# Kernel tuning notes

Measured on AMD Instinct MI355X. Metric: run time of the kernel, lower is better.

Reference implementation:

```python
import jax, jax.numpy as jnp
import numpy as np

N = 2_000_000
NUM_IN = 9
F1, F2 = 32, 64
NUM_SEG = 100_000
EPS = 1e-5


def setup_inputs() -> dict:
    key = jax.random.key(0)
    ks = jax.random.split(key, 10)
    points = jax.random.normal(ks[0], (N, NUM_IN), dtype=jnp.float32)
    inverse_indices = jax.random.randint(ks[1], (N,), 0, NUM_SEG, dtype=jnp.int64)
    w1 = jax.random.normal(ks[2], (NUM_IN, F1), dtype=jnp.float32) / np.sqrt(NUM_IN)
    b1 = jax.random.normal(ks[3], (F1,), dtype=jnp.float32) * 0.01
    g1 = jnp.ones((F1,), jnp.float32)
    be1 = jnp.zeros((F1,), jnp.float32)
    w2 = jax.random.normal(ks[4], (F1, F2), dtype=jnp.float32) / np.sqrt(F1)
    b2 = jax.random.normal(ks[5], (F2,), dtype=jnp.float32) * 0.01
    g2 = jnp.ones((F2,), jnp.float32)
    be2 = jnp.zeros((F2,), jnp.float32)
    return {
        "points": points, "inverse_indices": inverse_indices, "num_segments": NUM_SEG,
        "w1": w1, "b1": b1, "g1": g1, "be1": be1,
        "w2": w2, "b2": b2, "g2": g2, "be2": be2,
    }


def _linear_bn_relu(x, w, b, gamma, beta):
    # Linear -> BatchNorm1d (training-mode batch stats, biased var, eps=1e-5) -> ReLU
    h = x @ w + b
    mean = h.mean(axis=0)
    var = h.var(axis=0)  # biased, matches torch BN normalization
    h = (h - mean) * jax.lax.rsqrt(var + EPS) * gamma + beta
    return jax.nn.relu(h)


def reference(points, inverse_indices, num_segments, w1, b1, g1, be1, w2, b2, g2, be2):
    feat = _linear_bn_relu(points, w1, b1, g1, be1)
    feat = _linear_bn_relu(feat, w2, b2, g2, be2)
    # scatter_max over dim 0; torch_scatter zero-initializes empty segments,
    # and post-ReLU features are >= 0, so clamp -inf (empty) to 0.
    seg = jax.ops.segment_max(feat, inverse_indices, num_segments=num_segments)
    return jnp.maximum(seg, 0.0)
```

## Files before the change

kernel.cpp:

```cpp
#include <hip/hip_runtime.h>

#define EPS 1e-5f
#define NIN 9
#define F1 32
#define F2 64
#define NMOM 45
#define ROWB 80
#define SHIFT 7
#define NSEGB 128
#define NBMAX 1024
#define BT_MAIN 2048
#define BT_FB 8192
#define WSTRIDE 68

#define WS_S    0
#define WS_M    16
#define WS_S2   64
#define WS_SS2  128
#define WS_SC1  192
#define WS_SH1  224
#define WS_W1P  256
#define WS_SC2  544
#define WS_SH2  608

typedef __attribute__((ext_vector_type(8))) short bf16x8;
typedef __attribute__((ext_vector_type(4))) float f32x4;

__device__ __forceinline__ unsigned int f2bf(float f) {
    unsigned int u = __float_as_uint(f);
    return (u + 0x7fffu + ((u >> 16) & 1u)) >> 16;
}
__device__ __forceinline__ unsigned int pack2(float lo, float hi) {
    return f2bf(lo) | (f2bf(hi) << 16);
}

__global__ __launch_bounds__(256, 4) void moments_kernel(
    const float* __restrict__ pts, const int* __restrict__ idx,
    float* __restrict__ ws, int* __restrict__ histc, int N, int nb)
{
    __shared__ int lhist[NBMAX];
    __shared__ float red[64];
    for (int t = threadIdx.x; t < nb; t += 256) lhist[t] = 0;

    float S[NIN], M[NMOM];
#pragma unroll
    for (int k = 0; k < NIN; ++k) S[k] = 0.f;
#pragma unroll
    for (int m = 0; m < NMOM; ++m) M[m] = 0.f;
    __syncthreads();

    const int stride = gridDim.x * blockDim.x;
    for (int i = blockIdx.x * blockDim.x + threadIdx.x; i < N; i += stride) {
        const float* p = pts + (size_t)i * NIN;
        atomicAdd(&lhist[idx[i] >> SHIFT], 1);
        float x[NIN];
#pragma unroll
        for (int k = 0; k < NIN; ++k) x[k] = p[k];
        int m = 0;
#pragma unroll
        for (int k = 0; k < NIN; ++k) {
            S[k] += x[k];
#pragma unroll
            for (int l = k; l < NIN; ++l) { M[m] = fmaf(x[k], x[l], M[m]); ++m; }
        }
    }
#pragma unroll
    for (int off = 32; off > 0; off >>= 1) {
#pragma unroll
        for (int k = 0; k < NIN; ++k) S[k] += __shfl_xor(S[k], off, 64);
#pragma unroll
        for (int m = 0; m < NMOM; ++m) M[m] += __shfl_xor(M[m], off, 64);
    }
    if (threadIdx.x < 64) red[threadIdx.x] = 0.f;
    __syncthreads();
    if ((threadIdx.x & 63) == 0) {
#pragma unroll
        for (int k = 0; k < NIN; ++k) atomicAdd(&red[WS_S + k], S[k]);
#pragma unroll
        for (int m = 0; m < NMOM; ++m) atomicAdd(&red[WS_M + m], M[m]);
    }
    __syncthreads();
    if (threadIdx.x < 64) atomicAdd(&ws[threadIdx.x], red[threadIdx.x]);
    for (int t = threadIdx.x; t < nb; t += 256)
        if (lhist[t] > 0) atomicAdd(&histc[t], lhist[t]);
}

__global__ void scan_coarse_kernel(const int* __restrict__ histc,
                                   int* __restrict__ offsets,
                                   int* __restrict__ cursor, int nb)
{
    __shared__ int part[256];
    const int tid = threadIdx.x;
    int v[4];
    int sum = 0;
    const int base = tid * 4;
#pragma unroll
    for (int j = 0; j < 4; ++j) {
        const int i = base + j;
        v[j] = (i < nb) ? histc[i] : 0;
        sum += v[j];
    }
    part[tid] = sum;
    __syncthreads();
    for (int d = 1; d < 256; d <<= 1) {
        int t = (tid >= d) ? part[tid - d] : 0;
        __syncthreads();
        part[tid] += t;
        __syncthreads();
    }
    int pre = part[tid] - sum;
#pragma unroll
    for (int j = 0; j < 4; ++j) {
        const int i = base + j;
        if (i < nb) { offsets[i] = pre; cursor[i] = pre; }
        pre += v[j];
    }
    if (tid == 255) offsets[nb] = part[255];
}

__global__ void finalize1_kernel(
    const float* __restrict__ w1, const float* __restrict__ b1,
    const float* __restrict__ g1, const float* __restrict__ be1,
    float* __restrict__ ws, float invN)
{
    __shared__ float sc1s[F1];
    const int j = threadIdx.x;
    if (j < F1) {
        float W[NIN];
        float P = 0.f;
#pragma unroll
        for (int k = 0; k < NIN; ++k) {
            W[k] = w1[k * F1 + j];
            P = fmaf(ws[WS_S + k], W[k], P);
        }
        float Q = 0.f;
        int m = 0;
#pragma unroll
        for (int k = 0; k < NIN; ++k) {
            Q = fmaf(ws[WS_M + m], W[k] * W[k], Q); ++m;
#pragma unroll
            for (int l = k + 1; l < NIN; ++l) {
                Q = fmaf(2.f * ws[WS_M + m], W[k] * W[l], Q); ++m;
            }
        }
        const float b = b1[j];
        const float mean = fmaf(P, invN, b);
        const float Eh2 = fmaf(fmaf(2.f * b, P, Q), invN, b * b);
        const float var = Eh2 - mean * mean;
        const float sc = g1[j] * rsqrtf(var + EPS);
        ws[WS_SC1 + j] = sc;
        ws[WS_SH1 + j] = be1[j] - mean * sc;
        sc1s[j] = sc;
    }
    __syncthreads();
    for (int m = threadIdx.x; m < NIN * F1; m += blockDim.x)
        ws[WS_W1P + m] = w1[m] * sc1s[m & (F1 - 1)];
}

__global__ void finalize2_kernel(
    const float* __restrict__ g2, const float* __restrict__ be2,
    const float* __restrict__ b2, float* __restrict__ ws, float invN, float padf)
{
    const int j = threadIdx.x;
    if (j < F2) {
        const float b = b2[j];
        const float S  = ws[WS_S2 + j]  - padf * b;
        const float SS = ws[WS_SS2 + j] - padf * b * b;
        const float mean = S * invN;
        const float var  = SS * invN - mean * mean;
        const float sc   = g2[j] * rsqrtf(var + EPS);
        ws[WS_SC2 + j] = sc;
        ws[WS_SH2 + j] = be2[j] - mean * sc;
    }
}

__device__ __forceinline__ void f1_row_bf16(
    const float* __restrict__ p, const float* __restrict__ wl,
    const float* __restrict__ sh1, unsigned int* __restrict__ pk )
{
    float x[NIN];
#pragma unroll
    for (int k = 0; k < NIN; ++k) x[k] = p[k];
#pragma unroll
    for (int fc = 0; fc < 4; ++fc) {
        float h[8];
#pragma unroll
        for (int jj = 0; jj < 8; ++jj) h[jj] = sh1[fc * 8 + jj];
#pragma unroll
        for (int k = 0; k < NIN; ++k) {
            const float xv = x[k];
#pragma unroll
            for (int jj = 0; jj < 8; ++jj)
                h[jj] = fmaf(xv, wl[k * F1 + fc * 8 + jj], h[jj]);
        }
#pragma unroll
        for (int jj = 0; jj < 4; ++jj)
            pk[fc * 4 + jj] = pack2(fmaxf(h[2 * jj], 0.f), fmaxf(h[2 * jj + 1], 0.f));
    }
}

__global__ __launch_bounds__(256, 3) void binf1_kernel(
    const float* __restrict__ pts, const int* __restrict__ idx,
    const float* __restrict__ w2, const float* __restrict__ b2,
    float* __restrict__ ws, int* __restrict__ cursor,
    uint4* __restrict__ f1buf, int* __restrict__ fseg, int N, int nb)
{
    __shared__ int lcnt[NBMAX], runbase[NBMAX];
    __shared__ __align__(16) unsigned char stag[4][64 * ROWB];
    __shared__ float red[2 * F2];

    const int tid = threadIdx.x;
    const int t0 = blockIdx.x * BT_MAIN;
    const int lane = tid & 63, wv = tid >> 6;
    const int quad = lane >> 4, m16 = lane & 15;

    for (int t = tid; t < nb; t += 256) lcnt[t] = 0;
    __syncthreads();
#pragma unroll
    for (int r = 0; r < BT_MAIN / 256; ++r) {
        const int i = t0 + r * 256 + tid;
        if (i < N) atomicAdd(&lcnt[idx[i] >> SHIFT], 1);
    }
    __syncthreads();
    for (int t = tid; t < nb; t += 256) {
        const int c = lcnt[t];
        if (c > 0) runbase[t] = atomicAdd(&cursor[t], c);
        lcnt[t] = 0;
    }
    __syncthreads();

    bf16x8 bfr[4];
#pragma unroll
    for (int nt = 0; nt < 4; ++nt)
#pragma unroll
        for (int j = 0; j < 8; ++j)
            bfr[nt][j] = (short)f2bf(w2[(quad * 8 + j) * F2 + nt * 16 + m16]);
    float b2f[4];
#pragma unroll
    for (int nt = 0; nt < 4; ++nt) b2f[nt] = b2[nt * 16 + m16];

    const float* wl  = ws + WS_W1P;
    const float* sh1 = ws + WS_SH1;
    const f32x4 zero = {0.f, 0.f, 0.f, 0.f};
    float s[4] = {0.f, 0.f, 0.f, 0.f}, ss[4] = {0.f, 0.f, 0.f, 0.f};
    unsigned char* myst = stag[wv];

#pragma unroll 1
    for (int r = 0; r < BT_MAIN / 256; ++r) {
        const int cstart = t0 + r * 256 + wv * 64;
        if (cstart >= N) continue;
        const int i = cstart + lane;
        unsigned int pk[16];
        if (i < N) {
            f1_row_bf16(pts + (size_t)i * NIN, wl, sh1, pk);
        } else {
#pragma unroll
            for (int q = 0; q < 16; ++q) pk[q] = 0u;
        }
        uint4* wrow = (uint4*)(myst + lane * ROWB);
#pragma unroll
        for (int cidx = 0; cidx < 4; ++cidx)
            wrow[cidx] = make_uint4(pk[4*cidx+0], pk[4*cidx+1], pk[4*cidx+2], pk[4*cidx+3]);

        if (i < N) {
            const int sg = idx[i];
            const int bb = sg >> SHIFT;
            const int p = runbase[bb] + atomicAdd(&lcnt[bb], 1);
            uint4* dst = f1buf + (size_t)p * 4;
            dst[0] = make_uint4(pk[0],  pk[1],  pk[2],  pk[3]);
            dst[1] = make_uint4(pk[4],  pk[5],  pk[6],  pk[7]);
            dst[2] = make_uint4(pk[8],  pk[9],  pk[10], pk[11]);
            dst[3] = make_uint4(pk[12], pk[13], pk[14], pk[15]);
            fseg[p] = sg;
        }

        bf16x8 afr[4];
#pragma unroll
        for (int mt = 0; mt < 4; ++mt)
            afr[mt] = *(const bf16x8*)(myst + (mt * 16 + m16) * ROWB + quad * 16);
#pragma unroll
        for (int mt = 0; mt < 4; ++mt) {
#pragma unroll
            for (int nt = 0; nt < 4; ++nt) {
                f32x4 d = __builtin_amdgcn_mfma_f32_16x16x32_bf16(afr[mt], bfr[nt], zero, 0, 0, 0);
#pragma unroll
                for (int rr = 0; rr < 4; ++rr) {
                    const float v = d[rr] + b2f[nt];
                    s[nt] += v;
                    ss[nt] = fmaf(v, v, ss[nt]);
                }
            }
        }
    }

#pragma unroll
    for (int off = 16; off < 64; off <<= 1)
#pragma unroll
        for (int nt = 0; nt < 4; ++nt) {
            s[nt]  += __shfl_xor(s[nt], off, 64);
            ss[nt] += __shfl_xor(ss[nt], off, 64);
        }
    if (tid < 2 * F2) red[tid] = 0.f;
    __syncthreads();
    if (quad == 0) {
#pragma unroll
        for (int nt = 0; nt < 4; ++nt) {
            atomicAdd(&red[nt * 16 + m16], s[nt]);
            atomicAdd(&red[F2 + nt * 16 + m16], ss[nt]);
        }
    }
    __syncthreads();
    if (tid < F2) {
        atomicAdd(&ws[WS_S2 + tid],  red[tid]);
        atomicAdd(&ws[WS_SS2 + tid], red[F2 + tid]);
    }
}

__global__ __launch_bounds__(256, 3) void bucket_scatter_kernel(
    const uint4* __restrict__ f1buf, const int* __restrict__ fseg,
    const float* __restrict__ w2, const float* __restrict__ b2,
    const float* __restrict__ ws, const int* __restrict__ offsets,
    unsigned int* __restrict__ out, int nseg)
{
    __shared__ unsigned int win[NSEGB * WSTRIDE];
    __shared__ int segl[4][64];

    const int b = blockIdx.x;
    const int start = offsets[b], end = offsets[b + 1];
    const int tid = threadIdx.x;
    const int lane = tid & 63, wv = tid >> 6;
    const int quad = lane >> 4, m16 = lane & 15;

    for (int t = tid; t < NSEGB * WSTRIDE; t += 256) win[t] = 0u;

    bf16x8 bfr[4];
#pragma unroll
    for (int nt = 0; nt < 4; ++nt)
#pragma unroll
        for (int j = 0; j < 8; ++j)
            bfr[nt][j] = (short)f2bf(w2[(quad * 8 + j) * F2 + nt * 16 + m16]);
    float sc2f[4], shb[4];
#pragma unroll
    for (int nt = 0; nt < 4; ++nt) {
        const int f = nt * 16 + m16;
        sc2f[nt] = ws[WS_SC2 + f];
        shb[nt]  = fmaf(b2[f], sc2f[nt], ws[WS_SH2 + f]);
    }
    const f32x4 zero = {0.f, 0.f, 0.f, 0.f};
    __syncthreads();

    const int segbase = b << SHIFT;
    const int nch = (end - start + 63) >> 6;
    const bf16x8* fb = (const bf16x8*)f1buf;
    for (int c = wv; c < nch; c += 4) {
        const int cbase = start + c * 64;
        segl[wv][lane] = (cbase + lane < end) ? (fseg[cbase + lane] - segbase) : -1;
        bf16x8 afr[4];
#pragma unroll
        for (int mt = 0; mt < 4; ++mt) {
            const int ri = cbase + mt * 16 + m16;
            if (ri < end) {
                afr[mt] = fb[(size_t)ri * 4 + quad];
            } else {
#pragma unroll
                for (int j = 0; j < 8; ++j) afr[mt][j] = 0;
            }
        }
#pragma unroll
        for (int mt = 0; mt < 4; ++mt) {
            f32x4 d[4];
#pragma unroll
            for (int nt = 0; nt < 4; ++nt)
                d[nt] = __builtin_amdgcn_mfma_f32_16x16x32_bf16(afr[mt], bfr[nt], zero, 0, 0, 0);
#pragma unroll
            for (int rr = 0; rr < 4; ++rr) {
                const int sl = segl[wv][mt * 16 + quad * 4 + rr];
                if (sl >= 0) {
#pragma unroll
                    for (int nt = 0; nt < 4; ++nt) {
                        const float v = fmaf(d[nt][rr], sc2f[nt], shb[nt]);
                        if (v > 0.f)
                            atomicMax(&win[sl * WSTRIDE + nt * 16 + m16], __float_as_uint(v));
                    }
                }
            }
        }
    }
    __syncthreads();
    const int rows = min(NSEGB, nseg - segbase);
    for (int t = tid; t < rows * 64; t += 256)
        out[(size_t)(segbase + (t >> 6)) * 64 + (t & 63)] = win[(t >> 6) * WSTRIDE + (t & 63)];
}

__global__ __launch_bounds__(256) void binning_fb_kernel(
    const int* __restrict__ idx, int* __restrict__ cursor,
    int* __restrict__ sidx, int* __restrict__ fseg, int N, int nb)
{
    __shared__ int lcnt[NBMAX];
    __shared__ int runbase[NBMAX];
    const int tid = threadIdx.x;
    const int t0 = blockIdx.x * BT_FB;
    for (int t = tid; t < nb; t += 256) lcnt[t] = 0;
    __syncthreads();
#pragma unroll 4
    for (int r = 0; r < BT_FB / 256; ++r) {
        const int i = t0 + r * 256 + tid;
        if (i < N) atomicAdd(&lcnt[idx[i] >> SHIFT], 1);
    }
    __syncthreads();
    for (int t = tid; t < nb; t += 256) {
        const int c = lcnt[t];
        if (c > 0) runbase[t] = atomicAdd(&cursor[t], c);
        lcnt[t] = 0;
    }
    __syncthreads();
#pragma unroll 4
    for (int r = 0; r < BT_FB / 256; ++r) {
        const int i = t0 + r * 256 + tid;
        if (i < N) {
            const int sg = idx[i];
            const int bb = sg >> SHIFT;
            const int p = runbase[bb] + atomicAdd(&lcnt[bb], 1);
            sidx[p] = i;
            fseg[p] = sg;
        }
    }
}

__global__ __launch_bounds__(256, 3) void stats2_kernel(
    const float* __restrict__ pts, const float* __restrict__ w2,
    const float* __restrict__ b2, float* __restrict__ ws, int N)
{
    __shared__ __align__(16) unsigned char stag[4][64 * ROWB];
    __shared__ float red[2 * F2];

    const int lane = threadIdx.x & 63, wv = threadIdx.x >> 6;
    const int quad = lane >> 4, m16 = lane & 15;

    bf16x8 bfr[4];
#pragma unroll
    for (int nt = 0; nt < 4; ++nt)
#pragma unroll
        for (int j = 0; j < 8; ++j)
            bfr[nt][j] = (short)f2bf(w2[(quad * 8 + j) * F2 + nt * 16 + m16]);
    float b2f[4];
#pragma unroll
    for (int nt = 0; nt < 4; ++nt) b2f[nt] = b2[nt * 16 + m16];

    const float* wl  = ws + WS_W1P;
    const float* sh1 = ws + WS_SH1;
    const f32x4 zero = {0.f, 0.f, 0.f, 0.f};
    float s[4] = {0.f, 0.f, 0.f, 0.f}, ss[4] = {0.f, 0.f, 0.f, 0.f};

    unsigned char* myst = stag[wv];
    const int nchunks = (N + 63) / 64;
    for (int c = blockIdx.x * 4 + wv; c < nchunks; c += gridDim.x * 4) {
        const int i = c * 64 + lane;
        unsigned int pk[16];
        if (i < N) {
            f1_row_bf16(pts + (size_t)i * NIN, wl, sh1, pk);
        } else {
#pragma unroll
            for (int q = 0; q < 16; ++q) pk[q] = 0u;
        }
        uint4* wrow = (uint4*)(myst + lane * ROWB);
#pragma unroll
        for (int cidx = 0; cidx < 4; ++cidx)
            wrow[cidx] = make_uint4(pk[4*cidx+0], pk[4*cidx+1], pk[4*cidx+2], pk[4*cidx+3]);

        bf16x8 afr[4];
#pragma unroll
        for (int mt = 0; mt < 4; ++mt)
            afr[mt] = *(const bf16x8*)(myst + (mt * 16 + m16) * ROWB + quad * 16);
#pragma unroll
        for (int mt = 0; mt < 4; ++mt) {
#pragma unroll
            for (int nt = 0; nt < 4; ++nt) {
                f32x4 d = __builtin_amdgcn_mfma_f32_16x16x32_bf16(afr[mt], bfr[nt], zero, 0, 0, 0);
#pragma unroll
                for (int rr = 0; rr < 4; ++rr) {
                    const float v = d[rr] + b2f[nt];
                    s[nt] += v;
                    ss[nt] = fmaf(v, v, ss[nt]);
                }
            }
        }
    }
#pragma unroll
    for (int off = 16; off < 64; off <<= 1)
#pragma unroll
        for (int nt = 0; nt < 4; ++nt) {
            s[nt]  += __shfl_xor(s[nt], off, 64);
            ss[nt] += __shfl_xor(ss[nt], off, 64);
        }
    if (threadIdx.x < 2 * F2) red[threadIdx.x] = 0.f;
    __syncthreads();
    if (quad == 0) {
#pragma unroll
        for (int nt = 0; nt < 4; ++nt) {
            atomicAdd(&red[nt * 16 + m16], s[nt]);
            atomicAdd(&red[F2 + nt * 16 + m16], ss[nt]);
        }
    }
    __syncthreads();
    if (threadIdx.x < F2) {
        atomicAdd(&ws[WS_S2 + threadIdx.x],  red[threadIdx.x]);
        atomicAdd(&ws[WS_SS2 + threadIdx.x], red[F2 + threadIdx.x]);
    }
}

__global__ __launch_bounds__(256, 2) void bucket_scatter_gather_kernel(
    const float* __restrict__ pts, const int* __restrict__ sidx,
    const int* __restrict__ fseg, const float* __restrict__ w2,
    const float* __restrict__ b2, const float* __restrict__ ws,
    const int* __restrict__ offsets, unsigned int* __restrict__ out, int nseg)
{
    __shared__ unsigned int win[NSEGB * WSTRIDE];
    __shared__ __align__(16) unsigned char stag[4][64 * ROWB];
    __shared__ int segl[4][64];

    const int b = blockIdx.x;
    const int start = offsets[b], end = offsets[b + 1];
    const int tid = threadIdx.x;
    const int lane = tid & 63, wv = tid >> 6;
    const int quad = lane >> 4, m16 = lane & 15;

    for (int t = tid; t < NSEGB * WSTRIDE; t += 256) win[t] = 0u;

    bf16x8 bfr[4];
#pragma unroll
    for (int nt = 0; nt < 4; ++nt)
#pragma unroll
        for (int j = 0; j < 8; ++j)
            bfr[nt][j] = (short)f2bf(w2[(quad * 8 + j) * F2 + nt * 16 + m16]);
    float sc2f[4], shb[4];
#pragma unroll
    for (int nt = 0; nt < 4; ++nt) {
        const int f = nt * 16 + m16;
        sc2f[nt] = ws[WS_SC2 + f];
        shb[nt]  = fmaf(b2[f], sc2f[nt], ws[WS_SH2 + f]);
    }
    const float* wl  = ws + WS_W1P;
    const float* sh1 = ws + WS_SH1;
    const f32x4 zero = {0.f, 0.f, 0.f, 0.f};
    __syncthreads();

    const int segbase = b << SHIFT;
    const int nch = (end - start + 63) >> 6;
    unsigned char* myst = stag[wv];
    for (int c = wv; c < nch; c += 4) {
        const int cbase = start + c * 64;
        const int sp = cbase + lane;
        unsigned int pk[16];
        int sl = -1;
        if (sp < end) {
            f1_row_bf16(pts + (size_t)sidx[sp] * NIN, wl, sh1, pk);
            sl = fseg[sp] - segbase;
        } else {
#pragma unroll
            for (int q = 0; q < 16; ++q) pk[q] = 0u;
        }
        segl[wv][lane] = sl;
        uint4* wrow = (uint4*)(myst + lane * ROWB);
#pragma unroll
        for (int cidx = 0; cidx < 4; ++cidx)
            wrow[cidx] = make_uint4(pk[4*cidx+0], pk[4*cidx+1], pk[4*cidx+2], pk[4*cidx+3]);

        bf16x8 afr[4];
#pragma unroll
        for (int mt = 0; mt < 4; ++mt)
            afr[mt] = *(const bf16x8*)(myst + (mt * 16 + m16) * ROWB + quad * 16);
#pragma unroll
        for (int mt = 0; mt < 4; ++mt) {
            f32x4 d[4];
#pragma unroll
            for (int nt = 0; nt < 4; ++nt)
                d[nt] = __builtin_amdgcn_mfma_f32_16x16x32_bf16(afr[mt], bfr[nt], zero, 0, 0, 0);
#pragma unroll
            for (int rr = 0; rr < 4; ++rr) {
                const int sl2 = segl[wv][mt * 16 + quad * 4 + rr];
                if (sl2 >= 0) {
#pragma unroll
                    for (int nt = 0; nt < 4; ++nt) {
                        const float v = fmaf(d[nt][rr], sc2f[nt], shb[nt]);
                        if (v > 0.f)
                            atomicMax(&win[sl2 * WSTRIDE + nt * 16 + m16], __float_as_uint(v));
                    }
                }
            }
        }
    }
    __syncthreads();
    const int rows = min(NSEGB, nseg - segbase);
    for (int t = tid; t < rows * 64; t += 256)
        out[(size_t)(segbase + (t >> 6)) * 64 + (t & 63)] = win[(t >> 6) * WSTRIDE + (t & 63)];
}

extern "C" void kernel_launch(void* const* d_in, const int* in_sizes, int n_in,
                              void* d_out, int out_size, void* d_ws, size_t ws_size,
                              hipStream_t stream)
{
    const float* pts = (const float*)d_in[0];
    const int*   idx = (const int*)d_in[1];
    const float* w1  = (const float*)d_in[3];
    const float* b1  = (const float*)d_in[4];
    const float* g1  = (const float*)d_in[5];
    const float* be1 = (const float*)d_in[6];
    const float* w2  = (const float*)d_in[7];
    const float* b2  = (const float*)d_in[8];
    const float* g2  = (const float*)d_in[9];
    const float* be2 = (const float*)d_in[10];

    const int N = in_sizes[0] / NIN;
    const int nseg = out_size / F2;
    const int nb = (nseg + NSEGB - 1) >> SHIFT;
    const float invN = 1.0f / (float)N;
    const float padf = (float)((64 - (N & 63)) & 63);

    char* base = (char*)d_ws;
    const size_t f1bytes = (size_t)N * 64;
    const size_t need_main = f1bytes + 4096
                           + ((size_t)NBMAX + NBMAX + 1 + NBMAX + N) * sizeof(int) + 256;

    if (ws_size >= need_main) {
        uint4* f1buf   = (uint4*)base;
        float* ws      = (float*)(base + f1bytes);
        int*   histc   = (int*)(base + f1bytes + 4096);
        int*   offsets = histc + NBMAX;
        int*   cursor  = offsets + NBMAX + 1;
        int*   fseg    = cursor + NBMAX;

        hipMemsetAsync(ws, 0, 192 * sizeof(float), stream);
        hipMemsetAsync(histc, 0, NBMAX * sizeof(int), stream);

        moments_kernel<<<1024, 256, 0, stream>>>(pts, idx, ws, histc, N, nb);
        finalize1_kernel<<<1, 320, 0, stream>>>(w1, b1, g1, be1, ws, invN);
        scan_coarse_kernel<<<1, 256, 0, stream>>>(histc, offsets, cursor, nb);
        binf1_kernel<<<(N + BT_MAIN - 1) / BT_MAIN, 256, 0, stream>>>(
            pts, idx, w2, b2, ws, cursor, f1buf, fseg, N, nb);
        finalize2_kernel<<<1, 64, 0, stream>>>(g2, be2, b2, ws, invN, padf);
        bucket_scatter_kernel<<<nb, 256, 0, stream>>>(
            f1buf, fseg, w2, b2, ws, offsets, (unsigned int*)d_out, nseg);
    } else {
        float* ws      = (float*)base;
        int*   histc   = (int*)(base + 4096);
        int*   offsets = histc + NBMAX;
        int*   cursor  = offsets + NBMAX + 1;
        int*   sidx    = cursor + NBMAX;
        int*   fseg    = sidx + N;

        hipMemsetAsync(ws, 0, 192 * sizeof(float), stream);
        hipMemsetAsync(histc, 0, NBMAX * sizeof(int), stream);

        moments_kernel<<<1024, 256, 0, stream>>>(pts, idx, ws, histc, N, nb);
        finalize1_kernel<<<1, 320, 0, stream>>>(w1, b1, g1, be1, ws, invN);
        scan_coarse_kernel<<<1, 256, 0, stream>>>(histc, offsets, cursor, nb);
        binning_fb_kernel<<<(N + BT_FB - 1) / BT_FB, 256, 0, stream>>>(
            idx, cursor, sidx, fseg, N, nb);
        stats2_kernel<<<1024, 256, 0, stream>>>(pts, w2, b2, ws, N);
        finalize2_kernel<<<1, 64, 0, stream>>>(g2, be2, b2, ws, invN, padf);
        bucket_scatter_gather_kernel<<<nb, 256, 0, stream>>>(
            pts, sidx, fseg, w2, b2, ws, offsets, (unsigned int*)d_out, nseg);
    }
}
```

Measured before the change: 329.6 us.

## Split fused binning/F1 kernel into coalesced F1 write plus separate pair binning

The fused kernel that computed layer-1 features and scattered them into bucket order is split into two kernels. One writes bf16 F1 rows in original order with coalesced stores while accumulating layer-2 stats. The other bins (index, segment) pairs into a packed int2 array. The bucket scatter kernel now gathers F1 rows by index, so the scattered 64-byte writes become random 64-byte reads, plus an extra pass over idx and an extra launch.

```diff
diff --git a/kernel.cpp b/kernel.cpp
--- a/kernel.cpp
+++ b/kernel.cpp
@@ -9,8 +9,7 @@
 #define SHIFT 7
 #define NSEGB 128
 #define NBMAX 1024
-#define BT_MAIN 2048
-#define BT_FB 8192
+#define BT_BIN 8192
 #define WSTRIDE 68
 
 #define WS_S    0
@@ -199,237 +198,10 @@
     }
 }
 
-__global__ __launch_bounds__(256, 3) void binf1_kernel(
-    const float* __restrict__ pts, const int* __restrict__ idx,
-    const float* __restrict__ w2, const float* __restrict__ b2,
-    float* __restrict__ ws, int* __restrict__ cursor,
-    uint4* __restrict__ f1buf, int* __restrict__ fseg, int N, int nb)
-{
-    __shared__ int lcnt[NBMAX], runbase[NBMAX];
-    __shared__ __align__(16) unsigned char stag[4][64 * ROWB];
-    __shared__ float red[2 * F2];
-
-    const int tid = threadIdx.x;
-    const int t0 = blockIdx.x * BT_MAIN;
-    const int lane = tid & 63, wv = tid >> 6;
-    const int quad = lane >> 4, m16 = lane & 15;
-
-    for (int t = tid; t < nb; t += 256) lcnt[t] = 0;
-    __syncthreads();
-#pragma unroll
-    for (int r = 0; r < BT_MAIN / 256; ++r) {
-        const int i = t0 + r * 256 + tid;
-        if (i < N) atomicAdd(&lcnt[idx[i] >> SHIFT], 1);
-    }
-    __syncthreads();
-    for (int t = tid; t < nb; t += 256) {
-        const int c = lcnt[t];
-        if (c > 0) runbase[t] = atomicAdd(&cursor[t], c);
-        lcnt[t] = 0;
-    }
-    __syncthreads();
-
-    bf16x8 bfr[4];
-#pragma unroll
-    for (int nt = 0; nt < 4; ++nt)
-#pragma unroll
-        for (int j = 0; j < 8; ++j)
-            bfr[nt][j] = (short)f2bf(w2[(quad * 8 + j) * F2 + nt * 16 + m16]);
-    float b2f[4];
-#pragma unroll
-    for (int nt = 0; nt < 4; ++nt) b2f[nt] = b2[nt * 16 + m16];
-
-    const float* wl  = ws + WS_W1P;
-    const float* sh1 = ws + WS_SH1;
-    const f32x4 zero = {0.f, 0.f, 0.f, 0.f};
-    float s[4] = {0.f, 0.f, 0.f, 0.f}, ss[4] = {0.f, 0.f, 0.f, 0.f};
-    unsigned char* myst = stag[wv];
-
-#pragma unroll 1
-    for (int r = 0; r < BT_MAIN / 256; ++r) {
-        const int cstart = t0 + r * 256 + wv * 64;
-        if (cstart >= N) continue;
-        const int i = cstart + lane;
-        unsigned int pk[16];
-        if (i < N) {
-            f1_row_bf16(pts + (size_t)i * NIN, wl, sh1, pk);
-        } else {
-#pragma unroll
-            for (int q = 0; q < 16; ++q) pk[q] = 0u;
-        }
-        uint4* wrow = (uint4*)(myst + lane * ROWB);
-#pragma unroll
-        for (int cidx = 0; cidx < 4; ++cidx)
-            wrow[cidx] = make_uint4(pk[4*cidx+0], pk[4*cidx+1], pk[4*cidx+2], pk[4*cidx+3]);
-
-        if (i < N) {
-            const int sg = idx[i];
-            const int bb = sg >> SHIFT;
-            const int p = runbase[bb] + atomicAdd(&lcnt[bb], 1);
-            uint4* dst = f1buf + (size_t)p * 4;
-            dst[0] = make_uint4(pk[0],  pk[1],  pk[2],  pk[3]);
-            dst[1] = make_uint4(pk[4],  pk[5],  pk[6],  pk[7]);
-            dst[2] = make_uint4(pk[8],  pk[9],  pk[10], pk[11]);
-            dst[3] = make_uint4(pk[12], pk[13], pk[14], pk[15]);
-            fseg[p] = sg;
-        }
-
-        bf16x8 afr[4];
-#pragma unroll
-        for (int mt = 0; mt < 4; ++mt)
-            afr[mt] = *(const bf16x8*)(myst + (mt * 16 + m16) * ROWB + quad * 16);
-#pragma unroll
-        for (int mt = 0; mt < 4; ++mt) {
-#pragma unroll
-            for (int nt = 0; nt < 4; ++nt) {
-                f32x4 d = __builtin_amdgcn_mfma_f32_16x16x32_bf16(afr[mt], bfr[nt], zero, 0, 0, 0);
-#pragma unroll
-                for (int rr = 0; rr < 4; ++rr) {
-                    const float v = d[rr] + b2f[nt];
-                    s[nt] += v;
-                    ss[nt] = fmaf(v, v, ss[nt]);
-                }
-            }
-        }
-    }
-
-#pragma unroll
-    for (int off = 16; off < 64; off <<= 1)
-#pragma unroll
-        for (int nt = 0; nt < 4; ++nt) {
-            s[nt]  += __shfl_xor(s[nt], off, 64);
-            ss[nt] += __shfl_xor(ss[nt], off, 64);
-        }
-    if (tid < 2 * F2) red[tid] = 0.f;
-    __syncthreads();
-    if (quad == 0) {
-#pragma unroll
-        for (int nt = 0; nt < 4; ++nt) {
-            atomicAdd(&red[nt * 16 + m16], s[nt]);
-            atomicAdd(&red[F2 + nt * 16 + m16], ss[nt]);
-        }
-    }
-    __syncthreads();
-    if (tid < F2) {
-        atomicAdd(&ws[WS_S2 + tid],  red[tid]);
-        atomicAdd(&ws[WS_SS2 + tid], red[F2 + tid]);
-    }
-}
-
-__global__ __launch_bounds__(256, 3) void bucket_scatter_kernel(
-    const uint4* __restrict__ f1buf, const int* __restrict__ fseg,
-    const float* __restrict__ w2, const float* __restrict__ b2,
-    const float* __restrict__ ws, const int* __restrict__ offsets,
-    unsigned int* __restrict__ out, int nseg)
-{
-    __shared__ unsigned int win[NSEGB * WSTRIDE];
-    __shared__ int segl[4][64];
-
-    const int b = blockIdx.x;
-    const int start = offsets[b], end = offsets[b + 1];
-    const int tid = threadIdx.x;
-    const int lane = tid & 63, wv = tid >> 6;
-    const int quad = lane >> 4, m16 = lane & 15;
-
-    for (int t = tid; t < NSEGB * WSTRIDE; t += 256) win[t] = 0u;
-
-    bf16x8 bfr[4];
-#pragma unroll
-    for (int nt = 0; nt < 4; ++nt)
-#pragma unroll
-        for (int j = 0; j < 8; ++j)
-            bfr[nt][j] = (short)f2bf(w2[(quad * 8 + j) * F2 + nt * 16 + m16]);
-    float sc2f[4], shb[4];
-#pragma unroll
-    for (int nt = 0; nt < 4; ++nt) {
-        const int f = nt * 16 + m16;
-        sc2f[nt] = ws[WS_SC2 + f];
-        shb[nt]  = fmaf(b2[f], sc2f[nt], ws[WS_SH2 + f]);
-    }
-    const f32x4 zero = {0.f, 0.f, 0.f, 0.f};
-    __syncthreads();
-
-    const int segbase = b << SHIFT;
-    const int nch = (end - start + 63) >> 6;
-    const bf16x8* fb = (const bf16x8*)f1buf;
-    for (int c = wv; c < nch; c += 4) {
-        const int cbase = start + c * 64;
-        segl[wv][lane] = (cbase + lane < end) ? (fseg[cbase + lane] - segbase) : -1;
-        bf16x8 afr[4];
-#pragma unroll
-        for (int mt = 0; mt < 4; ++mt) {
-            const int ri = cbase + mt * 16 + m16;
-            if (ri < end) {
-                afr[mt] = fb[(size_t)ri * 4 + quad];
-            } else {
-#pragma unroll
-                for (int j = 0; j < 8; ++j) afr[mt][j] = 0;
-            }
-        }
-#pragma unroll
-        for (int mt = 0; mt < 4; ++mt) {
-            f32x4 d[4];
-#pragma unroll
-            for (int nt = 0; nt < 4; ++nt)
-                d[nt] = __builtin_amdgcn_mfma_f32_16x16x32_bf16(afr[mt], bfr[nt], zero, 0, 0, 0);
-#pragma unroll
-            for (int rr = 0; rr < 4; ++rr) {
-                const int sl = segl[wv][mt * 16 + quad * 4 + rr];
-                if (sl >= 0) {
-#pragma unroll
-                    for (int nt = 0; nt < 4; ++nt) {
-                        const float v = fmaf(d[nt][rr], sc2f[nt], shb[nt]);
-                        if (v > 0.f)
-                            atomicMax(&win[sl * WSTRIDE + nt * 16 + m16], __float_as_uint(v));
-                    }
-                }
-            }
-        }
-    }
-    __syncthreads();
-    const int rows = min(NSEGB, nseg - segbase);
-    for (int t = tid; t < rows * 64; t += 256)
-        out[(size_t)(segbase + (t >> 6)) * 64 + (t & 63)] = win[(t >> 6) * WSTRIDE + (t & 63)];
-}
-
-__global__ __launch_bounds__(256) void binning_fb_kernel(
-    const int* __restrict__ idx, int* __restrict__ cursor,
-    int* __restrict__ sidx, int* __restrict__ fseg, int N, int nb)
-{
-    __shared__ int lcnt[NBMAX];
-    __shared__ int runbase[NBMAX];
-    const int tid = threadIdx.x;
-    const int t0 = blockIdx.x * BT_FB;
-    for (int t = tid; t < nb; t += 256) lcnt[t] = 0;
-    __syncthreads();
-#pragma unroll 4
-    for (int r = 0; r < BT_FB / 256; ++r) {
-        const int i = t0 + r * 256 + tid;
-        if (i < N) atomicAdd(&lcnt[idx[i] >> SHIFT], 1);
-    }
-    __syncthreads();
-    for (int t = tid; t < nb; t += 256) {
-        const int c = lcnt[t];
-        if (c > 0) runbase[t] = atomicAdd(&cursor[t], c);
-        lcnt[t] = 0;
-    }
-    __syncthreads();
-#pragma unroll 4
-    for (int r = 0; r < BT_FB / 256; ++r) {
-        const int i = t0 + r * 256 + tid;
-        if (i < N) {
-            const int sg = idx[i];
-            const int bb = sg >> SHIFT;
-            const int p = runbase[bb] + atomicAdd(&lcnt[bb], 1);
-            sidx[p] = i;
-            fseg[p] = sg;
-        }
-    }
-}
-
-__global__ __launch_bounds__(256, 3) void stats2_kernel(
+__global__ __launch_bounds__(256, 3) void f1stats_kernel(
     const float* __restrict__ pts, const float* __restrict__ w2,
-    const float* __restrict__ b2, float* __restrict__ ws, int N)
+    const float* __restrict__ b2, float* __restrict__ ws,
+    uint4* __restrict__ f1buf, int N)
 {
     __shared__ __align__(16) unsigned char stag[4][64 * ROWB];
     __shared__ float red[2 * F2];
@@ -468,6 +240,14 @@
         for (int cidx = 0; cidx < 4; ++cidx)
             wrow[cidx] = make_uint4(pk[4*cidx+0], pk[4*cidx+1], pk[4*cidx+2], pk[4*cidx+3]);
 
+        if (i < N) {
+            uint4* dst = f1buf + (size_t)i * 4;
+            dst[0] = make_uint4(pk[0],  pk[1],  pk[2],  pk[3]);
+            dst[1] = make_uint4(pk[4],  pk[5],  pk[6],  pk[7]);
+            dst[2] = make_uint4(pk[8],  pk[9],  pk[10], pk[11]);
+            dst[3] = make_uint4(pk[12], pk[13], pk[14], pk[15]);
+        }
+
         bf16x8 afr[4];
 #pragma unroll
         for (int mt = 0; mt < 4; ++mt)
@@ -486,6 +266,7 @@
             }
         }
     }
+
 #pragma unroll
     for (int off = 16; off < 64; off <<= 1)
 #pragma unroll
@@ -509,11 +290,210 @@
     }
 }
 
+__global__ __launch_bounds__(256) void binning_kernel(
+    const int* __restrict__ idx, int* __restrict__ cursor,
+    int2* __restrict__ pair, int N, int nb)
+{
+    __shared__ int lcnt[NBMAX];
+    __shared__ int runbase[NBMAX];
+    const int tid = threadIdx.x;
+    const int t0 = blockIdx.x * BT_BIN;
+    for (int t = tid; t < nb; t += 256) lcnt[t] = 0;
+    __syncthreads();
+#pragma unroll 4
+    for (int r = 0; r < BT_BIN / 256; ++r) {
+        const int i = t0 + r * 256 + tid;
+        if (i < N) atomicAdd(&lcnt[idx[i] >> SHIFT], 1);
+    }
+    __syncthreads();
+    for (int t = tid; t < nb; t += 256) {
+        const int c = lcnt[t];
+        if (c > 0) runbase[t] = atomicAdd(&cursor[t], c);
+        lcnt[t] = 0;
+    }
+    __syncthreads();
+#pragma unroll 4
+    for (int r = 0; r < BT_BIN / 256; ++r) {
+        const int i = t0 + r * 256 + tid;
+        if (i < N) {
+            const int sg = idx[i];
+            const int bb = sg >> SHIFT;
+            const int p = runbase[bb] + atomicAdd(&lcnt[bb], 1);
+            pair[p] = make_int2(i, sg);
+        }
+    }
+}
+
+__global__ __launch_bounds__(256, 3) void bucket_scatter_kernel(
+    const uint4* __restrict__ f1buf, const int2* __restrict__ pair,
+    const float* __restrict__ w2, const float* __restrict__ b2,
+    const float* __restrict__ ws, const int* __restrict__ offsets,
+    unsigned int* __restrict__ out, int nseg)
+{
+    __shared__ unsigned int win[NSEGB * WSTRIDE];
+    __shared__ int2 prl[4][64];
+
+    const int b = blockIdx.x;
+    const int start = offsets[b], end = offsets[b + 1];
+    const int tid = threadIdx.x;
+    const int lane = tid & 63, wv = tid >> 6;
+    const int quad = lane >> 4, m16 = lane & 15;
+
+    for (int t = tid; t < NSEGB * WSTRIDE; t += 256) win[t] = 0u;
+
+    bf16x8 bfr[4];
+#pragma unroll
+    for (int nt = 0; nt < 4; ++nt)
+#pragma unroll
+        for (int j = 0; j < 8; ++j)
+            bfr[nt][j] = (short)f2bf(w2[(quad * 8 + j) * F2 + nt * 16 + m16]);
+    float sc2f[4], shb[4];
+#pragma unroll
+    for (int nt = 0; nt < 4; ++nt) {
+        const int f = nt * 16 + m16;
+        sc2f[nt] = ws[WS_SC2 + f];
+        shb[nt]  = fmaf(b2[f], sc2f[nt], ws[WS_SH2 + f]);
+    }
+    const f32x4 zero = {0.f, 0.f, 0.f, 0.f};
+    __syncthreads();
+
+    const int segbase = b << SHIFT;
+    const int nch = (end - start + 63) >> 6;
+    const bf16x8* fb = (const bf16x8*)f1buf;
+    for (int c = wv; c < nch; c += 4) {
+        const int cbase = start + c * 64;
+        const int sp = cbase + lane;
+        int2 pr = make_int2(0, -1);
+        if (sp < end) {
+            pr = pair[sp];
+            pr.y -= segbase;
+        }
+        prl[wv][lane] = pr;
+
+        bf16x8 afr[4];
+#pragma unroll
+        for (int mt = 0; mt < 4; ++mt) {
+            if (cbase + mt * 16 + m16 < end) {
+                const int gi = prl[wv][mt * 16 + m16].x;
+                afr[mt] = fb[(size_t)gi * 4 + quad];
+            } else {
+#pragma unroll
+                for (int j = 0; j < 8; ++j) afr[mt][j] = 0;
+            }
+        }
+#pragma unroll
+        for (int mt = 0; mt < 4; ++mt) {
+            f32x4 d[4];
+#pragma unroll
+            for (int nt = 0; nt < 4; ++nt)
+                d[nt] = __builtin_amdgcn_mfma_f32_16x16x32_bf16(afr[mt], bfr[nt], zero, 0, 0, 0);
+#pragma unroll
+            for (int rr = 0; rr < 4; ++rr) {
+                const int sl = prl[wv][mt * 16 + quad * 4 + rr].y;
+                if (sl >= 0) {
+#pragma unroll
+                    for (int nt = 0; nt < 4; ++nt) {
+                        const float v = fmaf(d[nt][rr], sc2f[nt], shb[nt]);
+                        if (v > 0.f)
+                            atomicMax(&win[sl * WSTRIDE + nt * 16 + m16], __float_as_uint(v));
+                    }
+                }
+            }
+        }
+    }
+    __syncthreads();
+    const int rows = min(NSEGB, nseg - segbase);
+    for (int t = tid; t < rows * 64; t += 256)
+        out[(size_t)(segbase + (t >> 6)) * 64 + (t & 63)] = win[(t >> 6) * WSTRIDE + (t & 63)];
+}
+
+__global__ __launch_bounds__(256, 3) void stats2_kernel(
+    const float* __restrict__ pts, const float* __restrict__ w2,
+    const float* __restrict__ b2, float* __restrict__ ws, int N)
+{
+    __shared__ __align__(16) unsigned char stag[4][64 * ROWB];
+    __shared__ float red[2 * F2];
+
+    const int lane = threadIdx.x & 63, wv = threadIdx.x >> 6;
+    const int quad = lane >> 4, m16 = lane & 15;
+
+    bf16x8 bfr[4];
+#pragma unroll
+    for (int nt = 0; nt < 4; ++nt)
+#pragma unroll
+        for (int j = 0; j < 8; ++j)
+            bfr[nt][j] = (short)f2bf(w2[(quad * 8 + j) * F2 + nt * 16 + m16]);
+    float b2f[4];
+#pragma unroll
+    for (int nt = 0; nt < 4; ++nt) b2f[nt] = b2[nt * 16 + m16];
+
+    const float* wl  = ws + WS_W1P;
+    const float* sh1 = ws + WS_SH1;
+    const f32x4 zero = {0.f, 0.f, 0.f, 0.f};
+    float s[4] = {0.f, 0.f, 0.f, 0.f}, ss[4] = {0.f, 0.f, 0.f, 0.f};
+
+    unsigned char* myst = stag[wv];
+    const int nchunks = (N + 63) / 64;
+    for (int c = blockIdx.x * 4 + wv; c < nchunks; c += gridDim.x * 4) {
+        const int i = c * 64 + lane;
+        unsigned int pk[16];
+        if (i < N) {
+            f1_row_bf16(pts + (size_t)i * NIN, wl, sh1, pk);
+        } else {
+#pragma unroll
+            for (int q = 0; q < 16; ++q) pk[q] = 0u;
+        }
+        uint4* wrow = (uint4*)(myst + lane * ROWB);
+#pragma unroll
+        for (int cidx = 0; cidx < 4; ++cidx)
+            wrow[cidx] = make_uint4(pk[4*cidx+0], pk[4*cidx+1], pk[4*cidx+2], pk[4*cidx+3]);
+
+        bf16x8 afr[4];
+#pragma unroll
+        for (int mt = 0; mt < 4; ++mt)
+            afr[mt] = *(const bf16x8*)(myst + (mt * 16 + m16) * ROWB + quad * 16);
+#pragma unroll
+        for (int mt = 0; mt < 4; ++mt) {
+#pragma unroll
+            for (int nt = 0; nt < 4; ++nt) {
+                f32x4 d = __builtin_amdgcn_mfma_f32_16x16x32_bf16(afr[mt], bfr[nt], zero, 0, 0, 0);
+#pragma unroll
+                for (int rr = 0; rr < 4; ++rr) {
+                    const float v = d[rr] + b2f[nt];
+                    s[nt] += v;
+                    ss[nt] = fmaf(v, v, ss[nt]);
+                }
+            }
+        }
+    }
+#pragma unroll
+    for (int off = 16; off < 64; off <<= 1)
+#pragma unroll
+        for (int nt = 0; nt < 4; ++nt) {
+            s[nt]  += __shfl_xor(s[nt], off, 64);
+            ss[nt] += __shfl_xor(ss[nt], off, 64);
+        }
+    if (threadIdx.x < 2 * F2) red[threadIdx.x] = 0.f;
+    __syncthreads();
+    if (quad == 0) {
+#pragma unroll
+        for (int nt = 0; nt < 4; ++nt) {
+            atomicAdd(&red[nt * 16 + m16], s[nt]);
+            atomicAdd(&red[F2 + nt * 16 + m16], ss[nt]);
+        }
+    }
+    __syncthreads();
+    if (threadIdx.x < F2) {
+        atomicAdd(&ws[WS_S2 + threadIdx.x],  red[threadIdx.x]);
+        atomicAdd(&ws[WS_SS2 + threadIdx.x], red[F2 + threadIdx.x]);
+    }
+}
+
 __global__ __launch_bounds__(256, 2) void bucket_scatter_gather_kernel(
-    const float* __restrict__ pts, const int* __restrict__ sidx,
-    const int* __restrict__ fseg, const float* __restrict__ w2,
-    const float* __restrict__ b2, const float* __restrict__ ws,
-    const int* __restrict__ offsets, unsigned int* __restrict__ out, int nseg)
+    const float* __restrict__ pts, const int2* __restrict__ pair,
+    const float* __restrict__ w2, const float* __restrict__ b2,
+    const float* __restrict__ ws, const int* __restrict__ offsets,
+    unsigned int* __restrict__ out, int nseg)
 {
     __shared__ unsigned int win[NSEGB * WSTRIDE];
     __shared__ __align__(16) unsigned char stag[4][64 * ROWB];
@@ -554,8 +534,9 @@
         unsigned int pk[16];
         int sl = -1;
         if (sp < end) {
-            f1_row_bf16(pts + (size_t)sidx[sp] * NIN, wl, sh1, pk);
-            sl = fseg[sp] - segbase;
+            const int2 pr = pair[sp];
+            f1_row_bf16(pts + (size_t)pr.x * NIN, wl, sh1, pk);
+            sl = pr.y - segbase;
         } else {
 #pragma unroll
             for (int q = 0; q < 16; ++q) pk[q] = 0u;
@@ -619,16 +600,17 @@
 
     char* base = (char*)d_ws;
     const size_t f1bytes = (size_t)N * 64;
-    const size_t need_main = f1bytes + 4096
-                           + ((size_t)NBMAX + NBMAX + 1 + NBMAX + N) * sizeof(int) + 256;
+    const size_t pairbytes = (size_t)N * 8;
+    const size_t tailbytes = 4096 + ((size_t)NBMAX + NBMAX + 1 + NBMAX) * sizeof(int) + 256;
+    const size_t need_main = f1bytes + pairbytes + tailbytes;
 
     if (ws_size >= need_main) {
         uint4* f1buf   = (uint4*)base;
-        float* ws      = (float*)(base + f1bytes);
-        int*   histc   = (int*)(base + f1bytes + 4096);
+        int2*  pair    = (int2*)(base + f1bytes);
+        float* ws      = (float*)(base + f1bytes + pairbytes);
+        int*   histc   = (int*)(base + f1bytes + pairbytes + 4096);
         int*   offsets = histc + NBMAX;
         int*   cursor  = offsets + NBMAX + 1;
-        int*   fseg    = cursor + NBMAX;
 
         hipMemsetAsync(ws, 0, 192 * sizeof(float), stream);
         hipMemsetAsync(histc, 0, NBMAX * sizeof(int), stream);
@@ -636,18 +618,18 @@
         moments_kernel<<<1024, 256, 0, stream>>>(pts, idx, ws, histc, N, nb);
         finalize1_kernel<<<1, 320, 0, stream>>>(w1, b1, g1, be1, ws, invN);
         scan_coarse_kernel<<<1, 256, 0, stream>>>(histc, offsets, cursor, nb);
-        binf1_kernel<<<(N + BT_MAIN - 1) / BT_MAIN, 256, 0, stream>>>(
-            pts, idx, w2, b2, ws, cursor, f1buf, fseg, N, nb);
+        f1stats_kernel<<<1024, 256, 0, stream>>>(pts, w2, b2, ws, f1buf, N);
+        binning_kernel<<<(N + BT_BIN - 1) / BT_BIN, 256, 0, stream>>>(
+            idx, cursor, pair, N, nb);
         finalize2_kernel<<<1, 64, 0, stream>>>(g2, be2, b2, ws, invN, padf);
         bucket_scatter_kernel<<<nb, 256, 0, stream>>>(
-            f1buf, fseg, w2, b2, ws, offsets, (unsigned int*)d_out, nseg);
+            f1buf, pair, w2, b2, ws, offsets, (unsigned int*)d_out, nseg);
     } else {
-        float* ws      = (float*)base;
-        int*   histc   = (int*)(base + 4096);
+        int2*  pair    = (int2*)base;
+        float* ws      = (float*)(base + pairbytes);
+        int*   histc   = (int*)(base + pairbytes + 4096);
         int*   offsets = histc + NBMAX;
         int*   cursor  = offsets + NBMAX + 1;
-        int*   sidx    = cursor + NBMAX;
-        int*   fseg    = sidx + N;
 
         hipMemsetAsync(ws, 0, 192 * sizeof(float), stream);
         hipMemsetAsync(histc, 0, NBMAX * sizeof(int), stream);
@@ -655,11 +637,11 @@
         moments_kernel<<<1024, 256, 0, stream>>>(pts, idx, ws, histc, N, nb);
         finalize1_kernel<<<1, 320, 0, stream>>>(w1, b1, g1, be1, ws, invN);
         scan_coarse_kernel<<<1, 256, 0, stream>>>(histc, offsets, cursor, nb);
-        binning_fb_kernel<<<(N + BT_FB - 1) / BT_FB, 256, 0, stream>>>(
-            idx, cursor, sidx, fseg, N, nb);
+        binning_kernel<<<(N + BT_BIN - 1) / BT_BIN, 256, 0, stream>>>(
+            idx, cursor, pair, N, nb);
         stats2_kernel<<<1024, 256, 0, stream>>>(pts, w2, b2, ws, N);
         finalize2_kernel<<<1, 64, 0, stream>>>(g2, be2, b2, ws, invN, padf);
         bucket_scatter_gather_kernel<<<nb, 256, 0, stream>>>(
-            pts, sidx, fseg, w2, b2, ws, offsets, (unsigned int*)d_out, nseg);
-    }
-}
+            pts, pair, w2, b2, ws, offsets, (unsigned int*)d_out, nseg);
+    }
+}
```

Measured after the change: 307.2 us. -6.8%, faster.
